# Kernel tuning notes

Measured on AMD Instinct MI355X. Metric: run time of the kernel, lower is better.

## Reference

```python
import jax, jax.numpy as jnp
import numpy as np

N, E = 10000, 160000
MUL0, MUL1, MUL2 = 64, 32, 16
DIM = MUL0 + MUL1 * 3 + MUL2 * 5          # 240
LAT, CPL, NTYPE = 128, 128, 95
NGATE = MUL1 + MUL2                        # 48 gate scalars
NCH = MUL0 + MUL1 + MUL2                   # 112 irrep channels
AVG_NEI = 16.0

# scaling_indices: per-channel index repeated over each irrep's dim
SCALE_IDX = np.concatenate([
    np.arange(MUL0),
    np.repeat(np.arange(MUL0, MUL0 + MUL1), 3),
    np.repeat(np.arange(MUL0 + MUL1, NCH), 5),
])


def _split(x, n):
    s = x[:, :MUL0]
    v1 = x[:, MUL0:MUL0 + MUL1 * 3].reshape(n, MUL1, 3)
    v2 = x[:, MUL0 + MUL1 * 3:].reshape(n, MUL2, 5)
    return s, v1, v2


def setup_inputs() -> dict:
    key = jax.random.key(0)
    ks = iter(jax.random.split(key, 48))
    rn = lambda *s: jax.random.normal(next(ks), s, dtype=jnp.float32)
    return dict(
        node_features=rn(N, DIM), edge_features=rn(E, DIM),
        latents=rn(E, LAT), msg_cpl=rn(N, CPL),
        node_onehot=jax.random.uniform(next(ks), (N, NTYPE), dtype=jnp.float32),
        wigner_D1=rn(E, 3, 3), wigner_D2=rn(E, 5, 5),
        so2_W0=rn(2 * MUL0, MUL0 + NGATE) * 0.08, so2_W1=rn(2 * MUL1, MUL1) * 0.12,
        so2_W2=rn(2 * MUL2, MUL2) * 0.17, so2_Ws=rn(LAT, NCH + NGATE) * 0.08,
        env_W=rn(LAT, NCH) * 0.08,
        post_W0=rn(MUL0, MUL0) * 0.12, post_b0=rn(MUL0) * 0.01,
        post_W1=rn(MUL1, MUL1) * 0.17, post_W2=rn(MUL2, MUL2) * 0.25,
        res_W0=rn(MUL0, MUL0) * 0.12, res_b0=rn(MUL0) * 0.01,
        res_W1=rn(MUL1, MUL1) * 0.17, res_W2=rn(MUL2, MUL2) * 0.25,
        cpl_W1=rn(CPL, CPL) * 0.08, cpl_b1=rn(CPL) * 0.01,
        cpl_W2=rn(CPL, NCH) * 0.08, cpl_b2=rn(NCH) * 0.01,
        gs_W=rn(MUL0, CPL) * 0.12, gs_b=rn(CPL) * 0.01,
        msg_W1=rn(2 * CPL, CPL) * 0.06, msg_b1=rn(CPL) * 0.01,
        msg_W2=rn(CPL, CPL) * 0.08, msg_b2=rn(CPL) * 0.01,
        ln_g=jnp.ones(CPL, jnp.float32), ln_b=jnp.zeros(CPL, jnp.float32),
        oh_w0=rn(MUL0, NTYPE) * 0.1, oh_w1=rn(MUL1, NTYPE) * 0.1, oh_w2=rn(MUL2, NTYPE) * 0.1,
        edge_index=jax.random.randint(next(ks), (2, E), 0, N),
    )


def _forward(node_features, edge_features, latents, msg_cpl, node_onehot,
             wigner_D1, wigner_D2, so2_W0, so2_W1, so2_W2, so2_Ws, env_W,
             post_W0, post_b0, post_W1, post_W2, res_W0, res_b0, res_W1, res_W2,
             cpl_W1, cpl_b1, cpl_W2, cpl_b2, gs_W, gs_b,
             msg_W1, msg_b1, msg_W2, msg_b2, ln_g, ln_b,
             oh_w0, oh_w1, oh_w2, edge_index):
    src = edge_index[0]
    ns, nv1, nv2 = _split(node_features, N)
    es, ev1, ev2 = _split(edge_features, E)
    # gather node feats to edges, concat with edge feats (per-l blocks)
    s_in = jnp.concatenate([ns[src], es], axis=1)                 # [E,128]
    v1_in = jnp.concatenate([nv1[src], ev1], axis=1)              # [E,64,3]
    v2_in = jnp.concatenate([nv2[src], ev2], axis=1)              # [E,32,5]
    # rotate into per-edge frame (Wigner D)
    v1_r = jnp.einsum('eij,ecj->eci', wigner_D1, v1_in)
    v2_r = jnp.einsum('eij,ecj->eci', wigner_D2, v2_in)
    # SO2 linear: shared channel mixing + latent-conditioned per-channel scales
    sc = latents @ so2_Ws                                         # [E,160]
    s_m = (s_in @ so2_W0) * sc[:, :MUL0 + NGATE]
    v1_m = jnp.einsum('eci,co->eoi', v1_r, so2_W1) * sc[:, MUL0 + NGATE:MUL0 + NGATE + MUL1, None]
    v2_m = jnp.einsum('eci,co->eoi', v2_r, so2_W2) * sc[:, MUL0 + NGATE + MUL1:, None]
    # rotate back
    v1_m = jnp.einsum('eji,eci->ecj', wigner_D1, v1_m)
    v2_m = jnp.einsum('eji,eci->ecj', wigner_D2, v2_m)
    # Gate activation
    s_act = jax.nn.silu(s_m[:, :MUL0])
    gates = jax.nn.sigmoid(s_m[:, MUL0:])
    v1_g = v1_m * gates[:, :MUL1, None]
    v2_g = v2_m * gates[:, MUL1:, None]
    # lin_post (per-l linear, bias on scalars)
    s_p = s_act @ post_W0 + post_b0
    v1_p = jnp.einsum('eci,co->eoi', v1_g, post_W1)
    v2_p = jnp.einsum('eci,co->eoi', v2_g, post_W2)
    # env element-wise weighting from latents
    w = latents @ env_W                                           # [E,112]
    s_p = s_p * w[:, :MUL0]
    v1_p = v1_p * w[:, MUL0:MUL0 + MUL1, None]
    v2_p = v2_p * w[:, MUL0 + MUL1:, None]
    msg = jnp.concatenate([s_p, v1_p.reshape(E, -1), v2_p.reshape(E, -1)], axis=1)
    # scatter-reduce to nodes + neighbor normalization
    agg = jax.ops.segment_sum(msg, src, num_segments=N) * (AVG_NEI ** -0.5)
    # coupling coefficients (per-channel, expanded by scaling_indices)
    coeffs = jax.nn.silu(msg_cpl @ cpl_W1 + cpl_b1) @ cpl_W2 + cpl_b2
    new_nf = agg * coeffs[:, SCALE_IDX]
    # coupling-channel update
    scal = new_nf[:, :MUL0] @ gs_W + gs_b
    h = jnp.concatenate([scal, msg_cpl], axis=1)
    upd = jax.nn.silu(h @ msg_W1 + msg_b1) @ msg_W2 + msg_b2
    mc = msg_cpl + upd
    mu = mc.mean(-1, keepdims=True)
    var = mc.var(-1, keepdims=True)
    msg_cpl_out = (mc - mu) * jax.lax.rsqrt(var + 1e-5) * ln_g + ln_b
    # residual mix with fixed logit-0 coefficients
    c = jax.nn.sigmoid(jnp.float32(0.0))
    c_old = jax.lax.rsqrt(c * c + 1.0)
    c_new = c * c_old
    rs = ns @ res_W0 + res_b0
    rv1 = jnp.einsum('eci,co->eoi', nv1, res_W1)
    rv2 = jnp.einsum('eci,co->eoi', nv2, res_W2)
    res = jnp.concatenate([rs, rv1.reshape(N, -1), rv2.reshape(N, -1)], axis=1)
    nf = c_new * new_nf + c_old * res
    # layer one-hot tensor product ('uvu' with 95x0e)
    inv = 1.0 / np.sqrt(NTYPE).astype(np.float32)
    g0 = (node_onehot @ oh_w0.T) * inv
    g1 = (node_onehot @ oh_w1.T) * inv
    g2 = (node_onehot @ oh_w2.T) * inv
    os_, ov1, ov2 = _split(nf, N)
    oh = jnp.concatenate([os_ * g0, (ov1 * g1[:, :, None]).reshape(N, -1),
                          (ov2 * g2[:, :, None]).reshape(N, -1)], axis=1)
    return nf + oh, msg_cpl_out


def reference(node_features, edge_features, latents, msg_cpl, node_onehot,
              wigner_D1, wigner_D2, so2_W0, so2_W1, so2_W2, so2_Ws, env_W,
              post_W0, post_b0, post_W1, post_W2, res_W0, res_b0, res_W1, res_W2,
              cpl_W1, cpl_b1, cpl_W2, cpl_b2, gs_W, gs_b,
              msg_W1, msg_b1, msg_W2, msg_b2, ln_g, ln_b,
              oh_w0, oh_w1, oh_w2, edge_index):
    return _forward(node_features, edge_features, latents, msg_cpl, node_onehot,
                    wigner_D1, wigner_D2, so2_W0, so2_W1, so2_W2, so2_Ws, env_W,
                    post_W0, post_b0, post_W1, post_W2, res_W0, res_b0, res_W1, res_W2,
                    cpl_W1, cpl_b1, cpl_W2, cpl_b2, gs_W, gs_b,
                    msg_W1, msg_b1, msg_W2, msg_b2, ln_g, ln_b,
                    oh_w0, oh_w1, oh_w2, edge_index)
```

## Files before the change

### kernel.cpp

```cpp
#include <hip/hip_runtime.h>

#define NN   10000
#define NE   160000
#define DIM  240
#define EB   16
#define NPB  16

typedef __bf16 bf16x8 __attribute__((ext_vector_type(8)));
typedef __bf16 bf16x4 __attribute__((ext_vector_type(4)));
typedef float  f32x4  __attribute__((ext_vector_type(4)));

__device__ __forceinline__ float sigf(float x) { return 1.0f / (1.0f + __expf(-x)); }

#define OFF_WB1 0
#define OFF_WB2 34816
#define OFF_W1  49152
#define OFF_W2  51200
#define OFF_PW0 51712
#define OFF_PW1 55808
#define OFF_PW2 56832
#define OHT_BYTE_OFF 131072
#define CNT_BYTE_OFF 196608
#define ROW_BYTE_OFF 237568
#define CUR_BYTE_OFF 282624
#define EID_BYTE_OFF 327680

__global__ __launch_bounds__(256) void prep_kernel(
    const float* __restrict__ Ws, const float* __restrict__ We, const float* __restrict__ W0,
    const float* __restrict__ W1, const float* __restrict__ W2,
    const float* __restrict__ pW0, const float* __restrict__ pW1, const float* __restrict__ pW2,
    const float* __restrict__ w0g, const float* __restrict__ w1g, const float* __restrict__ w2g,
    __bf16* __restrict__ wsb, float* __restrict__ ohT,
    const int* __restrict__ src, int* __restrict__ cnt)
{
    if (blockIdx.x >= 56) {
        if (cnt) {
            int e = (blockIdx.x - 56) * 256 + threadIdx.x;
            if (e < NE) atomicAdd(&cnt[src[e]], 1);
        }
        return;
    }
    int tid = blockIdx.x * 256 + threadIdx.x;
    const int stride = 56 * 256;
    for (int idx = tid; idx < 17*4*512; idx += stride) {
        int j = idx & 7, lane = (idx >> 3) & 63, ks = (idx >> 9) & 3, nt = idx >> 11;
        int k = ks*32 + (lane >> 4)*8 + j, n = nt*16 + (lane & 15);
        float v = (n < 160) ? Ws[k*160 + n] : We[k*112 + (n - 160)];
        wsb[OFF_WB1 + idx] = (__bf16)v;
    }
    for (int idx = tid; idx < 7*4*512; idx += stride) {
        int j = idx & 7, lane = (idx >> 3) & 63, ks = (idx >> 9) & 3, nt = idx >> 11;
        int k = ks*32 + (lane >> 4)*8 + j, n = nt*16 + (lane & 15);
        wsb[OFF_WB2 + idx] = (__bf16)W0[k*112 + n];
    }
    for (int idx = tid; idx < 2*2*512; idx += stride) {
        int j = idx & 7, lane = (idx >> 3) & 63, ks = (idx >> 9) & 1, nt = idx >> 10;
        int k = ks*32 + (lane >> 4)*8 + j, n = nt*16 + (lane & 15);
        wsb[OFF_W1 + idx] = (__bf16)W1[k*32 + n];
    }
    for (int idx = tid; idx < 512; idx += stride) {
        int j = idx & 7, lane = (idx >> 3) & 63;
        int k = (lane >> 4)*8 + j, n = lane & 15;
        wsb[OFF_W2 + idx] = (__bf16)W2[k*16 + n];
    }
    for (int idx = tid; idx < 4*2*512; idx += stride) {
        int j = idx & 7, lane = (idx >> 3) & 63, ks = (idx >> 9) & 1, nt = idx >> 10;
        int k = ks*32 + (lane >> 4)*8 + j, n = nt*16 + (lane & 15);
        wsb[OFF_PW0 + idx] = (__bf16)pW0[k*64 + n];
    }
    for (int idx = tid; idx < 2*512; idx += stride) {
        int j = idx & 7, lane = (idx >> 3) & 63, nt = idx >> 9;
        int k = (lane >> 4)*8 + j, n = nt*16 + (lane & 15);
        wsb[OFF_PW1 + idx] = (__bf16)pW1[k*32 + n];
    }
    for (int idx = tid; idx < 512; idx += stride) {
        int j = idx & 7, lane = (idx >> 3) & 63;
        int k = (lane >> 4)*8 + j, n = lane & 15;
        wsb[OFF_PW2 + idx] = (k < 16) ? (__bf16)pW2[k*16 + n] : (__bf16)0.0f;
    }
    for (int idx = tid; idx < 96*112; idx += stride) {
        int k = idx / 112, n2 = idx - k*112;
        float v = 0.f;
        if (k < 95) {
            if (n2 < 64)      v = w0g[n2*95 + k];
            else if (n2 < 96) v = w1g[(n2-64)*95 + k];
            else              v = w2g[(n2-96)*95 + k];
        }
        ohT[idx] = v * 0.10259783521f;
    }
}

__global__ __launch_bounds__(256) void scan_kernel(const int* __restrict__ cnt,
                                                   int* __restrict__ rowptr, int* __restrict__ cur) {
    __shared__ int part[256];
    int t = threadIdx.x;
    int base = t * 40;
    int local[40];
    int s = 0;
    #pragma unroll
    for (int i = 0; i < 40; i++) {
        int idx = base + i;
        int v = (idx < NN) ? cnt[idx] : 0;
        local[i] = s; s += v;
    }
    part[t] = s;
    __syncthreads();
    for (int off = 1; off < 256; off <<= 1) {
        int v = (t >= off) ? part[t - off] : 0;
        __syncthreads();
        part[t] += v;
        __syncthreads();
    }
    int pre = (t > 0) ? part[t - 1] : 0;
    #pragma unroll
    for (int i = 0; i < 40; i++) {
        int idx = base + i;
        if (idx < NN) { int r = pre + local[i]; rowptr[idx] = r; cur[idx] = r; }
    }
    if (t == 255) rowptr[NN] = part[255];
}

__global__ __launch_bounds__(256) void fill_kernel(const int* __restrict__ src,
                                                   int* __restrict__ cur, int* __restrict__ eidl) {
    int e = blockIdx.x * 256 + threadIdx.x;
    if (e < NE) {
        int slot = atomicAdd(&cur[src[e]], 1);
        eidl[slot] = e;
    }
}

__global__ __launch_bounds__(256, 4) void edge_mfma_kernel(
    const float* __restrict__ nf, const float* __restrict__ ef,
    const float* __restrict__ latg, const float* __restrict__ D1g, const float* __restrict__ D2g,
    const float* __restrict__ pb0, const int* __restrict__ srcg,
    const int* __restrict__ eidl, const __bf16* __restrict__ wsb, float* agg)
{
    __shared__ __align__(16) unsigned char pool[39936];
    __bf16* Cb   = (__bf16*)(pool + 0);
    __bf16* v1m  = (__bf16*)(pool + 12544);
    __bf16* v2m  = (__bf16*)(pool + 16384);
    __bf16* mtile= (__bf16*)(pool + 12544);
    __bf16* vt1  = (__bf16*)(pool + 20736);
    __bf16* vt2  = (__bf16*)(pool + 27136);
    __bf16* aV1g = (__bf16*)(pool + 20736);
    __bf16* aV2g = (__bf16*)(pool + 23808);
    float*  d1s  = (float*)(pool + 32512);
    float*  d2s  = (float*)(pool + 33088);
    __bf16* aSact= (__bf16*)(pool + 35648);
    float*  e1s  = (float*)(pool + 37696);
    float*  e2s  = (float*)(pool + 38272);
    int*    srcs = (int*)  (pool + 39872);

    const int t    = threadIdx.x;
    const int wid  = t >> 6, lane = t & 63;
    const int e0   = blockIdx.x * EB;

    #define EIDX(e) (eidl ? eidl[e0 + (e)] : (e0 + (e)))

    if (t < 16) srcs[t] = srcg[EIDX(t)];

    for (int idx = t; idx < 144; idx += 256) {
        int e = idx / 9; int ee = EIDX(e);
        d1s[idx] = D1g[(size_t)ee*9 + (idx - e*9)];
    }
    for (int idx = t; idx < 400; idx += 256) {
        int e = idx / 25; int ee = EIDX(e);
        d2s[idx] = D2g[(size_t)ee*25 + (idx - e*25)];
    }
    {
        int e = t >> 4, half = (t >> 3) & 1, cq = t & 7;
        int ee = EIDX(e);
        const float* base = half ? (ef + (size_t)ee*240 + 64 + cq*12)
                                 : (nf + (size_t)srcg[ee]*240 + 64 + cq*12);
        float4 f0 = *(const float4*)base;
        float4 f1 = *(const float4*)(base + 4);
        float4 f2 = *(const float4*)(base + 8);
        float f[12] = {f0.x,f0.y,f0.z,f0.w,f1.x,f1.y,f1.z,f1.w,f2.x,f2.y,f2.z,f2.w};
        int c = half*32 + cq*4;
        __bf16* dst = vt1 + e*200 + c;
        #pragma unroll
        for (int i = 0; i < 3; i++) {
            bf16x4 v = {(__bf16)f[i], (__bf16)f[3+i], (__bf16)f[6+i], (__bf16)f[9+i]};
            *(bf16x4*)(dst + i*64) = v;
        }
    }
    if (t < 128) {
        int e = t >> 3, half = (t >> 2) & 1, cq = t & 3;
        int ee = EIDX(e);
        const float* base = half ? (ef + (size_t)ee*240 + 160 + cq*20)
                                 : (nf + (size_t)srcg[ee]*240 + 160 + cq*20);
        float f[20];
        #pragma unroll
        for (int k = 0; k < 5; k++) {
            float4 q4 = *(const float4*)(base + k*4);
            f[4*k] = q4.x; f[4*k+1] = q4.y; f[4*k+2] = q4.z; f[4*k+3] = q4.w;
        }
        int c = half*16 + cq*4;
        __bf16* dst = vt2 + e*168 + c;
        #pragma unroll
        for (int z = 0; z < 5; z++) {
            bf16x4 v = {(__bf16)f[z], (__bf16)f[5+z], (__bf16)f[10+z], (__bf16)f[15+z]};
            *(bf16x4*)(dst + z*32) = v;
        }
    }

    {
        int col16 = lane & 15, ebase = (lane >> 4)*4;
        int e = lane & 15, q = lane >> 4;
        int ee = EIDX(e); int sn = srcg[ee];
        const float* latp = latg + (size_t)ee*128 + q*8;
        const float* nfp  = nf  + (size_t)sn*240 + q*8;
        const float* efp  = ef  + (size_t)ee*240 + q*8;
        bf16x8 aL[4], aS[4];
        #pragma unroll
        for (int ks = 0; ks < 4; ks++) {
            float4 f0 = *(const float4*)(latp + ks*32);
            float4 f1 = *(const float4*)(latp + ks*32 + 4);
            bf16x8 v;
            v[0]=(__bf16)f0.x; v[1]=(__bf16)f0.y; v[2]=(__bf16)f0.z; v[3]=(__bf16)f0.w;
            v[4]=(__bf16)f1.x; v[5]=(__bf16)f1.y; v[6]=(__bf16)f1.z; v[7]=(__bf16)f1.w;
            aL[ks] = v;
            const float* sp = (ks < 2) ? (nfp + ks*32) : (efp + (ks - 2)*32);
            float4 g0 = *(const float4*)sp;
            float4 g1 = *(const float4*)(sp + 4);
            bf16x8 w;
            w[0]=(__bf16)g0.x; w[1]=(__bf16)g0.y; w[2]=(__bf16)g0.z; w[3]=(__bf16)g0.w;
            w[4]=(__bf16)g1.x; w[5]=(__bf16)g1.y; w[6]=(__bf16)g1.z; w[7]=(__bf16)g1.w;
            aS[ks] = w;
        }
        #pragma unroll
        for (int it = 0; it < 6; it++) {
            int nt = wid + it*4;
            bool isLat = nt < 17;
            const __bf16* bB = isLat ? (wsb + OFF_WB1 + nt*2048)
                                     : (wsb + OFF_WB2 + (nt - 17)*2048);
            f32x4 acc = {0.f, 0.f, 0.f, 0.f};
            #pragma unroll
            for (int ks = 0; ks < 4; ks++) {
                bf16x8 b = *(const bf16x8*)(bB + (ks*64 + lane)*8);
                acc = __builtin_amdgcn_mfma_f32_16x16x32_bf16(isLat ? aL[ks] : aS[ks], b, acc, 0, 0, 0);
            }
            int col = (isLat ? nt*16 : 272 + (nt - 17)*16) + col16;
            #pragma unroll
            for (int r = 0; r < 4; r++) Cb[(ebase + r)*392 + col] = (__bf16)acc[r];
        }
    }
    __syncthreads();

    {
        int col16 = lane & 15, er = lane & 15, q8 = (lane >> 4)*8, ebase = (lane >> 4)*4;
        for (int p = wid; p < 11; p += 4) {
            f32x4 acc = {0.f, 0.f, 0.f, 0.f};
            if (p < 6) {
                int i = p >> 1, nt = p & 1;
                #pragma unroll
                for (int ks = 0; ks < 2; ks++) {
                    bf16x8 a = *(const bf16x8*)(vt1 + er*200 + i*64 + ks*32 + q8);
                    bf16x8 b = *(const bf16x8*)(wsb + OFF_W1 + ((nt*2 + ks)*64 + lane)*8);
                    acc = __builtin_amdgcn_mfma_f32_16x16x32_bf16(a, b, acc, 0, 0, 0);
                }
                int col = nt*16 + col16;
                #pragma unroll
                for (int r = 0; r < 4; r++) v1m[(i*16 + ebase + r)*40 + col] = (__bf16)acc[r];
            } else {
                int i = p - 6;
                bf16x8 a = *(const bf16x8*)(vt2 + er*168 + i*32 + q8);
                bf16x8 b = *(const bf16x8*)(wsb + OFF_W2 + lane*8);
                acc = __builtin_amdgcn_mfma_f32_16x16x32_bf16(a, b, acc, 0, 0, 0);
                #pragma unroll
                for (int r = 0; r < 4; r++) v2m[(i*16 + ebase + r)*24 + col16] = (__bf16)acc[r];
            }
        }
    }
    if (t < 128) {
        int ks = t >> 6, l2 = t & 63, e = l2 & 15, o0 = ks*32 + (l2 >> 4)*8;
        bf16x8 v;
        #pragma unroll
        for (int j = 0; j < 8; j++) {
            int o = o0 + j;
            float x = (float)Cb[e*392 + 272 + o] * (float)Cb[e*392 + o];
            v[j] = (__bf16)(x * sigf(x));
        }
        *(bf16x8*)(aSact + t*8) = v;
    }
    for (int idx = t; idx < 544; idx += 256) {
        if (idx < 144) {
            int e = idx / 9, r = idx - e*9, i = r / 3, k = r - i*3;
            const float* d = d1s + e*9;
            e1s[idx] = d[i*3+0]*d[0*3+k] + d[i*3+1]*d[1*3+k] + d[i*3+2]*d[2*3+k];
        } else {
            int j = idx - 144;
            int e = j / 25, r = j - e*25, i = r / 5, k = r - i*5;
            const float* d = d2s + e*25;
            float a = 0.f;
            #pragma unroll
            for (int tt = 0; tt < 5; tt++) a += d[i*5+tt] * d[tt*5+k];
            e2s[j] = a;
        }
    }
    __syncthreads();

    for (int idx = t; idx < 512; idx += 256) {
        if (idx < 192) {
            int i = idx >> 6, l2 = idx & 63, e = l2 & 15, c0 = (l2 >> 4)*8;
            float z0 = e1s[e*9 + i*3], z1 = e1s[e*9 + i*3 + 1], z2 = e1s[e*9 + i*3 + 2];
            bf16x8 m0 = *(const bf16x8*)(v1m + (0*16 + e)*40 + c0);
            bf16x8 m1 = *(const bf16x8*)(v1m + (1*16 + e)*40 + c0);
            bf16x8 m2 = *(const bf16x8*)(v1m + (2*16 + e)*40 + c0);
            bf16x8 s8 = *(const bf16x8*)(Cb + e*392 + 112 + c0);
            bf16x8 gA = *(const bf16x8*)(Cb + e*392 + 336 + c0);
            bf16x8 gB = *(const bf16x8*)(Cb + e*392 + 64 + c0);
            bf16x8 v;
            #pragma unroll
            for (int j = 0; j < 8; j++) {
                float g = sigf((float)gA[j] * (float)gB[j]);
                float a = z0*(float)m0[j] + z1*(float)m1[j] + z2*(float)m2[j];
                v[j] = (__bf16)(g * (float)s8[j] * a);
            }
            *(bf16x8*)(aV1g + idx*8) = v;
        } else {
            int idx2 = idx - 192;
            int i = idx2 >> 6, l2 = idx2 & 63, e = l2 & 15, c0 = (l2 >> 4)*8;
            bf16x8 v;
            if (c0 < 16) {
                const float* ee = e2s + e*25 + i*5;
                float z0 = ee[0], z1 = ee[1], z2 = ee[2], z3 = ee[3], z4 = ee[4];
                bf16x8 m0 = *(const bf16x8*)(v2m + (0*16 + e)*24 + c0);
                bf16x8 m1 = *(const bf16x8*)(v2m + (1*16 + e)*24 + c0);
                bf16x8 m2 = *(const bf16x8*)(v2m + (2*16 + e)*24 + c0);
                bf16x8 m3 = *(const bf16x8*)(v2m + (3*16 + e)*24 + c0);
                bf16x8 m4 = *(const bf16x8*)(v2m + (4*16 + e)*24 + c0);
                bf16x8 s8 = *(const bf16x8*)(Cb + e*392 + 144 + c0);
                bf16x8 gA = *(const bf16x8*)(Cb + e*392 + 368 + c0);
                bf16x8 gB = *(const bf16x8*)(Cb + e*392 + 96 + c0);
                #pragma unroll
                for (int j = 0; j < 8; j++) {
                    float g = sigf((float)gA[j] * (float)gB[j]);
                    float a = z0*(float)m0[j] + z1*(float)m1[j] + z2*(float)m2[j]
                            + z3*(float)m3[j] + z4*(float)m4[j];
                    v[j] = (__bf16)(g * (float)s8[j] * a);
                }
            } else {
                #pragma unroll
                for (int j = 0; j < 8; j++) v[j] = (__bf16)0.0f;
            }
            *(bf16x8*)(aV2g + idx2*8) = v;
        }
    }
    __syncthreads();

    {
        int col16 = lane & 15, ebase = (lane >> 4)*4;
        for (int p = wid; p < 15; p += 4) {
            f32x4 acc = {0.f, 0.f, 0.f, 0.f};
            if (p < 4) {
                int nt = p;
                #pragma unroll
                for (int ks = 0; ks < 2; ks++) {
                    bf16x8 a = *(const bf16x8*)(aSact + (ks*64 + lane)*8);
                    bf16x8 b = *(const bf16x8*)(wsb + OFF_PW0 + ((nt*2 + ks)*64 + lane)*8);
                    acc = __builtin_amdgcn_mfma_f32_16x16x32_bf16(a, b, acc, 0, 0, 0);
                }
                int o = nt*16 + col16;
                float bias = pb0[o];
                #pragma unroll
                for (int r = 0; r < 4; r++) {
                    int e = ebase + r;
                    float val = (acc[r] + bias) * (float)Cb[e*392 + 160 + o];
                    if (eidl) mtile[e*248 + o] = (__bf16)val;
                    else      atomicAdd(agg + (size_t)srcs[e]*240 + o, val);
                }
            } else if (p < 10) {
                int q = p - 4, i = q >> 1, nt = q & 1;
                bf16x8 a = *(const bf16x8*)(aV1g + (i*64 + lane)*8);
                bf16x8 b = *(const bf16x8*)(wsb + OFF_PW1 + (nt*64 + lane)*8);
                acc = __builtin_amdgcn_mfma_f32_16x16x32_bf16(a, b, acc, 0, 0, 0);
                int o = nt*16 + col16;
                #pragma unroll
                for (int r = 0; r < 4; r++) {
                    int e = ebase + r;
                    float val = acc[r] * (float)Cb[e*392 + 224 + o];
                    if (eidl) mtile[e*248 + 64 + o*3 + i] = (__bf16)val;
                    else      atomicAdd(agg + (size_t)srcs[e]*240 + 64 + o*3 + i, val);
                }
            } else {
                int i = p - 10;
                bf16x8 a = *(const bf16x8*)(aV2g + (i*64 + lane)*8);
                bf16x8 b = *(const bf16x8*)(wsb + OFF_PW2 + lane*8);
                acc = __builtin_amdgcn_mfma_f32_16x16x32_bf16(a, b, acc, 0, 0, 0);
                #pragma unroll
                for (int r = 0; r < 4; r++) {
                    int e = ebase + r;
                    float val = acc[r] * (float)Cb[e*392 + 256 + col16];
                    if (eidl) mtile[e*248 + 160 + col16*5 + i] = (__bf16)val;
                    else      atomicAdd(agg + (size_t)srcs[e]*240 + 160 + col16*5 + i, val);
                }
            }
        }
    }

    if (eidl) {
        __syncthreads();
        if (t < 240) {
            float s = 0.f;
            int prev = srcs[0];
            #pragma unroll
            for (int e = 0; e < EB; e++) {
                int sn = srcs[e];
                if (sn != prev) {
                    atomicAdd(agg + (size_t)prev*240 + t, s);
                    s = 0.f; prev = sn;
                }
                s += (float)mtile[e*248 + t];
            }
            atomicAdd(agg + (size_t)prev*240 + t, s);
        }
    }
    #undef EIDX
}

__global__ __launch_bounds__(256, 3) void node_kernel(
    const float* __restrict__ nf, const float* __restrict__ mcplg,
    const float* __restrict__ ohg,
    const float* __restrict__ cW1, const float* __restrict__ cb1,
    const float* __restrict__ cW2, const float* __restrict__ cb2,
    const float* __restrict__ gsW, const float* __restrict__ gsb,
    const float* __restrict__ mW1, const float* __restrict__ mb1,
    const float* __restrict__ mW2, const float* __restrict__ mb2,
    const float* __restrict__ lng, const float* __restrict__ lnb,
    const float* __restrict__ rW0, const float* __restrict__ rb0,
    const float* __restrict__ rW1, const float* __restrict__ rW2,
    const float* __restrict__ ohT, float* out0, float* out1)
{
    __shared__ __align__(16) unsigned char pool[53248];
    float* mcp  = (float*)(pool + 0);
    float* ohv  = (float*)(pool + 8192);
    float* anew = (float*)(pool + 14336);
    float* t12  = (float*)(pool + 29696);
    float* cfg  = (float*)(pool + 37888);
    float* scm  = (float*)(pool + 45056);

    const int t  = threadIdx.x;
    const int g  = t >> 7;
    const int o  = t & 127;
    const int nb = g * 8;
    const int n0 = blockIdx.x * NPB;

    for (int idx = t; idx < NPB * 128; idx += 256) {
        int n = idx >> 7, k = idx & 127;
        mcp[n*128 + k] = mcplg[(n0 + n) * 128 + k];
    }
    for (int idx = t; idx < NPB * 96; idx += 256) {
        int n = idx / 96, k = idx - n * 96;
        ohv[n*96 + k] = (k < 95) ? ohg[(n0 + n) * 95 + k] : 0.f;
    }
    for (int idx = t; idx < NPB * 240; idx += 256) {
        int n = idx / 240, k = idx - n * 240;
        anew[n*240 + k] = out0[(n0 + n) * DIM + k];
    }
    __syncthreads();

    {
        float a[8]; float b = cb1[o];
        #pragma unroll
        for (int i = 0; i < 8; i++) a[i] = b;
        #pragma unroll 2
        for (int k4 = 0; k4 < 32; k4++) {
            float w0 = cW1[(4*k4+0)*128 + o], w1 = cW1[(4*k4+1)*128 + o],
                  w2 = cW1[(4*k4+2)*128 + o], w3 = cW1[(4*k4+3)*128 + o];
            #pragma unroll
            for (int i = 0; i < 8; i++) {
                float4 m = *(const float4*)&mcp[(nb+i)*128 + 4*k4];
                a[i] += m.x*w0 + m.y*w1 + m.z*w2 + m.w*w3;
            }
        }
        #pragma unroll
        for (int i = 0; i < 8; i++) { float x = a[i]; t12[(nb+i)*128 + o] = x * sigf(x); }
    }
    __syncthreads();

    if (o < 112) {
        float a[8]; float b = cb2[o];
        #pragma unroll
        for (int i = 0; i < 8; i++) a[i] = b;
        #pragma unroll 2
        for (int k4 = 0; k4 < 32; k4++) {
            float w0 = cW2[(4*k4+0)*112 + o], w1 = cW2[(4*k4+1)*112 + o],
                  w2 = cW2[(4*k4+2)*112 + o], w3 = cW2[(4*k4+3)*112 + o];
            #pragma unroll
            for (int i = 0; i < 8; i++) {
                float4 m = *(const float4*)&t12[(nb+i)*128 + 4*k4];
                a[i] += m.x*w0 + m.y*w1 + m.z*w2 + m.w*w3;
            }
        }
        #pragma unroll
        for (int i = 0; i < 8; i++) cfg[(nb+i)*112 + o] = a[i];
    }
    __syncthreads();

    for (int idx = t; idx < NPB * 240; idx += 256) {
        int n = idx / 240, d = idx - n * 240;
        int ch = (d < 64) ? d : (d < 160 ? 64 + (d - 64) / 3 : 96 + (d - 160) / 5);
        anew[n*240 + d] *= 0.25f * cfg[n*112 + ch];
    }
    __syncthreads();

    {
        float a[8]; float b = gsb[o];
        #pragma unroll
        for (int i = 0; i < 8; i++) a[i] = b;
        #pragma unroll 2
        for (int k4 = 0; k4 < 16; k4++) {
            float w0 = gsW[(4*k4+0)*128 + o], w1 = gsW[(4*k4+1)*128 + o],
                  w2 = gsW[(4*k4+2)*128 + o], w3 = gsW[(4*k4+3)*128 + o];
            #pragma unroll
            for (int i = 0; i < 8; i++) {
                float4 m = *(const float4*)&anew[(nb+i)*240 + 4*k4];
                a[i] += m.x*w0 + m.y*w1 + m.z*w2 + m.w*w3;
            }
        }
        #pragma unroll
        for (int i = 0; i < 8; i++) scm[(nb+i)*128 + o] = a[i];
    }
    __syncthreads();

    {
        float a[8]; float b = mb1[o];
        #pragma unroll
        for (int i = 0; i < 8; i++) a[i] = b;
        #pragma unroll 2
        for (int k4 = 0; k4 < 32; k4++) {
            float w0 = mW1[(4*k4+0)*128 + o], w1 = mW1[(4*k4+1)*128 + o],
                  w2 = mW1[(4*k4+2)*128 + o], w3 = mW1[(4*k4+3)*128 + o];
            #pragma unroll
            for (int i = 0; i < 8; i++) {
                float4 m = *(const float4*)&scm[(nb+i)*128 + 4*k4];
                a[i] += m.x*w0 + m.y*w1 + m.z*w2 + m.w*w3;
            }
        }
        #pragma unroll 2
        for (int k4 = 0; k4 < 32; k4++) {
            float w0 = mW1[(128+4*k4+0)*128 + o], w1 = mW1[(128+4*k4+1)*128 + o],
                  w2 = mW1[(128+4*k4+2)*128 + o], w3 = mW1[(128+4*k4+3)*128 + o];
            #pragma unroll
            for (int i = 0; i < 8; i++) {
                float4 m = *(const float4*)&mcp[(nb+i)*128 + 4*k4];
                a[i] += m.x*w0 + m.y*w1 + m.z*w2 + m.w*w3;
            }
        }
        #pragma unroll
        for (int i = 0; i < 8; i++) { float x = a[i]; t12[(nb+i)*128 + o] = x * sigf(x); }
    }
    __syncthreads();

    {
        float a[8]; float b = mb2[o];
        #pragma unroll
        for (int i = 0; i < 8; i++) a[i] = b;
        #pragma unroll 2
        for (int k4 = 0; k4 < 32; k4++) {
            float w0 = mW2[(4*k4+0)*128 + o], w1 = mW2[(4*k4+1)*128 + o],
                  w2 = mW2[(4*k4+2)*128 + o], w3 = mW2[(4*k4+3)*128 + o];
            #pragma unroll
            for (int i = 0; i < 8; i++) {
                float4 m = *(const float4*)&t12[(nb+i)*128 + 4*k4];
                a[i] += m.x*w0 + m.y*w1 + m.z*w2 + m.w*w3;
            }
        }
        #pragma unroll
        for (int i = 0; i < 8; i++) scm[(nb+i)*128 + o] = mcp[(nb+i)*128 + o] + a[i];
    }
    __syncthreads();

    {
        int n = t >> 4, l = t & 15;
        float x[8]; float s = 0.f, ss = 0.f;
        #pragma unroll
        for (int i = 0; i < 8; i++) { x[i] = scm[n*128 + l + 16*i]; s += x[i]; ss += x[i]*x[i]; }
        #pragma unroll
        for (int off = 8; off > 0; off >>= 1) {
            s  += __shfl_down(s,  off, 16);
            ss += __shfl_down(ss, off, 16);
        }
        s  = __shfl(s, 0, 16);
        ss = __shfl(ss, 0, 16);
        float mu   = s * (1.f / 128.f);
        float var  = ss * (1.f / 128.f) - mu * mu;
        float rstd = rsqrtf(var + 1e-5f);
        float* op = out1 + (n0 + n) * 128;
        #pragma unroll
        for (int i = 0; i < 8; i++) {
            int c = l + 16*i;
            op[c] = (x[i] - mu) * rstd * lng[c] + lnb[c];
        }
    }

    if (o < 112) {
        float a[8] = {0.f,0.f,0.f,0.f,0.f,0.f,0.f,0.f};
        #pragma unroll 2
        for (int k4 = 0; k4 < 24; k4++) {
            float w0 = ohT[(4*k4+0)*112 + o], w1 = ohT[(4*k4+1)*112 + o],
                  w2 = ohT[(4*k4+2)*112 + o], w3 = ohT[(4*k4+3)*112 + o];
            #pragma unroll
            for (int i = 0; i < 8; i++) {
                float4 m = *(const float4*)&ohv[(nb+i)*96 + 4*k4];
                a[i] += m.x*w0 + m.y*w1 + m.z*w2 + m.w*w3;
            }
        }
        #pragma unroll
        for (int i = 0; i < 8; i++) cfg[(nb+i)*112 + o] = a[i];
    }
    __syncthreads();

    const float c_new = 0.4472135955f;
    const float c_old = 0.8944271910f;
    for (int idx = t; idx < NPB * 240; idx += 256) {
        int n = idx / 240, d = idx - n * 240;
        const float* nrow = nf + (size_t)(n0 + n) * DIM;
        float res, gg;
        if (d < 64) {
            float acc = rb0[d];
            #pragma unroll 4
            for (int c = 0; c < 64; c++) acc += nrow[c] * rW0[c * 64 + d];
            res = acc; gg = cfg[n*112 + d];
        } else if (d < 160) {
            int dd = d - 64, oo = dd / 3, j = dd - oo * 3;
            float acc = 0.f;
            #pragma unroll 4
            for (int c = 0; c < 32; c++) acc += nrow[64 + c*3 + j] * rW1[c * 32 + oo];
            res = acc; gg = cfg[n*112 + 64 + oo];
        } else {
            int dd = d - 160, oo = dd / 5, j = dd - oo * 5;
            float acc = 0.f;
            #pragma unroll 4
            for (int c = 0; c < 16; c++) acc += nrow[160 + c*5 + j] * rW2[c * 16 + oo];
            res = acc; gg = cfg[n*112 + 96 + oo];
        }
        float v = c_new * anew[n*240 + d] + c_old * res;
        out0[(n0 + n) * DIM + d] = v * (1.f + gg);
    }
}

extern "C" void kernel_launch(void* const* d_in, const int* in_sizes, int n_in,
                              void* d_out, int out_size, void* d_ws, size_t ws_size,
                              hipStream_t stream) {
    const float* nf      = (const float*)d_in[0];
    const float* ef      = (const float*)d_in[1];
    const float* lat     = (const float*)d_in[2];
    const float* mcpl    = (const float*)d_in[3];
    const float* ohot    = (const float*)d_in[4];
    const float* D1      = (const float*)d_in[5];
    const float* D2      = (const float*)d_in[6];
    const float* so2_W0  = (const float*)d_in[7];
    const float* so2_W1  = (const float*)d_in[8];
    const float* so2_W2  = (const float*)d_in[9];
    const float* so2_Ws  = (const float*)d_in[10];
    const float* env_W   = (const float*)d_in[11];
    const float* post_W0 = (const float*)d_in[12];
    const float* post_b0 = (const float*)d_in[13];
    const float* post_W1 = (const float*)d_in[14];
    const float* post_W2 = (const float*)d_in[15];
    const float* res_W0  = (const float*)d_in[16];
    const float* res_b0  = (const float*)d_in[17];
    const float* res_W1  = (const float*)d_in[18];
    const float* res_W2  = (const float*)d_in[19];
    const float* cpl_W1  = (const float*)d_in[20];
    const float* cpl_b1  = (const float*)d_in[21];
    const float* cpl_W2  = (const float*)d_in[22];
    const float* cpl_b2  = (const float*)d_in[23];
    const float* gs_W    = (const float*)d_in[24];
    const float* gs_b    = (const float*)d_in[25];
    const float* msg_W1  = (const float*)d_in[26];
    const float* msg_b1  = (const float*)d_in[27];
    const float* msg_W2  = (const float*)d_in[28];
    const float* msg_b2  = (const float*)d_in[29];
    const float* ln_g    = (const float*)d_in[30];
    const float* ln_b    = (const float*)d_in[31];
    const float* oh_w0   = (const float*)d_in[32];
    const float* oh_w1   = (const float*)d_in[33];
    const float* oh_w2   = (const float*)d_in[34];
    const int*   eidx    = (const int*)d_in[35];

    float* out0 = (float*)d_out;
    float* out1 = (float*)d_out + (size_t)NN * DIM;
    char*   wsB = (char*)d_ws;
    __bf16* wsb = (__bf16*)d_ws;
    float*  ohT = (float*)(wsB + OHT_BYTE_OFF);

    const size_t needA = (size_t)EID_BYTE_OFF + (size_t)NE * sizeof(int);
    const bool planA = ws_size >= needA;

    (void)hipMemsetAsync(out0, 0, (size_t)NN * DIM * sizeof(float), stream);

    if (planA) {
        int* cnt  = (int*)(wsB + CNT_BYTE_OFF);
        int* row  = (int*)(wsB + ROW_BYTE_OFF);
        int* cur  = (int*)(wsB + CUR_BYTE_OFF);
        int* eidl = (int*)(wsB + EID_BYTE_OFF);

        (void)hipMemsetAsync(cnt, 0, 10240 * sizeof(int), stream);
        prep_kernel<<<56 + (NE + 255) / 256, 256, 0, stream>>>(
            so2_Ws, env_W, so2_W0, so2_W1, so2_W2, post_W0, post_W1, post_W2,
            oh_w0, oh_w1, oh_w2, wsb, ohT, eidx, cnt);
        scan_kernel<<<1, 256, 0, stream>>>(cnt, row, cur);
        fill_kernel<<<(NE + 255) / 256, 256, 0, stream>>>(eidx, cur, eidl);

        edge_mfma_kernel<<<NE / EB, 256, 0, stream>>>(
            nf, ef, lat, D1, D2, post_b0, eidx, eidl, wsb, out0);
    } else {
        prep_kernel<<<56, 256, 0, stream>>>(
            so2_Ws, env_W, so2_W0, so2_W1, so2_W2, post_W0, post_W1, post_W2,
            oh_w0, oh_w1, oh_w2, wsb, ohT, eidx, nullptr);
        edge_mfma_kernel<<<NE / EB, 256, 0, stream>>>(
            nf, ef, lat, D1, D2, post_b0, eidx, nullptr, wsb, out0);
    }

    node_kernel<<<NN / NPB, 256, 0, stream>>>(
        nf, mcpl, ohot, cpl_W1, cpl_b1, cpl_W2, cpl_b2, gs_W, gs_b,
        msg_W1, msg_b1, msg_W2, msg_b2, ln_g, ln_b,
        res_W0, res_b0, res_W1, res_W2, ohT, out0, out1);
}
```

Before: 689.2 us.

## Halve edge tile to 8 edges per block with 128-thread blocks

```diff
diff --git a/kernel.cpp b/kernel.cpp
--- a/kernel.cpp
+++ b/kernel.cpp
@@ -3,7 +3,7 @@
 #define NN   10000
 #define NE   160000
 #define DIM  240
-#define EB   16
+#define EB   8
 #define NPB  16
 
 typedef __bf16 bf16x8 __attribute__((ext_vector_type(8)));
@@ -129,27 +129,27 @@
     }
 }
 
-__global__ __launch_bounds__(256, 4) void edge_mfma_kernel(
+__global__ __launch_bounds__(128, 4) void edge_mfma_kernel(
     const float* __restrict__ nf, const float* __restrict__ ef,
     const float* __restrict__ latg, const float* __restrict__ D1g, const float* __restrict__ D2g,
     const float* __restrict__ pb0, const int* __restrict__ srcg,
     const int* __restrict__ eidl, const __bf16* __restrict__ wsb, float* agg)
 {
-    __shared__ __align__(16) unsigned char pool[39936];
+    __shared__ __align__(16) unsigned char pool[20384];
     __bf16* Cb   = (__bf16*)(pool + 0);
-    __bf16* v1m  = (__bf16*)(pool + 12544);
-    __bf16* v2m  = (__bf16*)(pool + 16384);
-    __bf16* mtile= (__bf16*)(pool + 12544);
-    __bf16* vt1  = (__bf16*)(pool + 20736);
-    __bf16* vt2  = (__bf16*)(pool + 27136);
-    __bf16* aV1g = (__bf16*)(pool + 20736);
-    __bf16* aV2g = (__bf16*)(pool + 23808);
-    float*  d1s  = (float*)(pool + 32512);
-    float*  d2s  = (float*)(pool + 33088);
-    __bf16* aSact= (__bf16*)(pool + 35648);
-    float*  e1s  = (float*)(pool + 37696);
-    float*  e2s  = (float*)(pool + 38272);
-    int*    srcs = (int*)  (pool + 39872);
+    __bf16* v1m  = (__bf16*)(pool + 6272);
+    __bf16* v2m  = (__bf16*)(pool + 8192);
+    __bf16* mtile= (__bf16*)(pool + 6272);
+    __bf16* vt1  = (__bf16*)(pool + 10240);
+    __bf16* vt2  = (__bf16*)(pool + 13440);
+    __bf16* aV1g = (__bf16*)(pool + 10240);
+    __bf16* aV2g = (__bf16*)(pool + 13312);
+    float*  d1s  = (float*)(pool + 16128);
+    float*  d2s  = (float*)(pool + 16416);
+    float*  e1s  = (float*)(pool + 17216);
+    float*  e2s  = (float*)(pool + 17504);
+    __bf16* aSact= (__bf16*)(pool + 18304);
+    int*    srcs = (int*)  (pool + 20352);
 
     const int t    = threadIdx.x;
     const int wid  = t >> 6, lane = t & 63;
@@ -157,15 +157,15 @@
 
     #define EIDX(e) (eidl ? eidl[e0 + (e)] : (e0 + (e)))
 
-    if (t < 16) srcs[t] = srcg[EIDX(t)];
-
-    for (int idx = t; idx < 144; idx += 256) {
-        int e = idx / 9; int ee = EIDX(e);
-        d1s[idx] = D1g[(size_t)ee*9 + (idx - e*9)];
-    }
-    for (int idx = t; idx < 400; idx += 256) {
-        int e = idx / 25; int ee = EIDX(e);
-        d2s[idx] = D2g[(size_t)ee*25 + (idx - e*25)];
+    if (t < 8) srcs[t] = srcg[EIDX(t)];
+
+    for (int idx = t; idx < 72; idx += 128) {
+        int e = idx / 9;
+        d1s[idx] = D1g[(size_t)EIDX(e)*9 + (idx - e*9)];
+    }
+    for (int idx = t; idx < 200; idx += 128) {
+        int e = idx / 25;
+        d2s[idx] = D2g[(size_t)EIDX(e)*25 + (idx - e*25)];
     }
     {
         int e = t >> 4, half = (t >> 3) & 1, cq = t & 7;
@@ -184,7 +184,7 @@
             *(bf16x4*)(dst + i*64) = v;
         }
     }
-    if (t < 128) {
+    if (t < 64) {
         int e = t >> 3, half = (t >> 2) & 1, cq = t & 3;
         int ee = EIDX(e);
         const float* base = half ? (ef + (size_t)ee*240 + 160 + cq*20)
@@ -206,8 +206,8 @@
 
     {
         int col16 = lane & 15, ebase = (lane >> 4)*4;
-        int e = lane & 15, q = lane >> 4;
-        int ee = EIDX(e); int sn = srcg[ee];
+        int er = lane & 7, q = lane >> 4;
+        int ee = EIDX(er); int sn = srcg[ee];
         const float* latp = latg + (size_t)ee*128 + q*8;
         const float* nfp  = nf  + (size_t)sn*240 + q*8;
         const float* efp  = ef  + (size_t)ee*240 + q*8;
@@ -228,9 +228,9 @@
             w[4]=(__bf16)g1.x; w[5]=(__bf16)g1.y; w[6]=(__bf16)g1.z; w[7]=(__bf16)g1.w;
             aS[ks] = w;
         }
-        #pragma unroll
-        for (int it = 0; it < 6; it++) {
-            int nt = wid + it*4;
+        #pragma unroll 4
+        for (int it = 0; it < 12; it++) {
+            int nt = wid + it*2;
             bool isLat = nt < 17;
             const __bf16* bB = isLat ? (wsb + OFF_WB1 + nt*2048)
                                      : (wsb + OFF_WB2 + (nt - 17)*2048);
@@ -240,16 +240,18 @@
                 bf16x8 b = *(const bf16x8*)(bB + (ks*64 + lane)*8);
                 acc = __builtin_amdgcn_mfma_f32_16x16x32_bf16(isLat ? aL[ks] : aS[ks], b, acc, 0, 0, 0);
             }
-            int col = (isLat ? nt*16 : 272 + (nt - 17)*16) + col16;
-            #pragma unroll
-            for (int r = 0; r < 4; r++) Cb[(ebase + r)*392 + col] = (__bf16)acc[r];
-        }
-    }
-    __syncthreads();
-
-    {
-        int col16 = lane & 15, er = lane & 15, q8 = (lane >> 4)*8, ebase = (lane >> 4)*4;
-        for (int p = wid; p < 11; p += 4) {
+            if (ebase < 8) {
+                int col = (isLat ? nt*16 : 272 + (nt - 17)*16) + col16;
+                #pragma unroll
+                for (int r = 0; r < 4; r++) Cb[(ebase + r)*392 + col] = (__bf16)acc[r];
+            }
+        }
+    }
+    __syncthreads();
+
+    {
+        int col16 = lane & 15, er = lane & 7, q8 = (lane >> 4)*8, ebase = (lane >> 4)*4;
+        for (int p = wid; p < 11; p += 2) {
             f32x4 acc = {0.f, 0.f, 0.f, 0.f};
             if (p < 6) {
                 int i = p >> 1, nt = p & 1;
@@ -259,21 +261,25 @@
                     bf16x8 b = *(const bf16x8*)(wsb + OFF_W1 + ((nt*2 + ks)*64 + lane)*8);
                     acc = __builtin_amdgcn_mfma_f32_16x16x32_bf16(a, b, acc, 0, 0, 0);
                 }
-                int col = nt*16 + col16;
-                #pragma unroll
-                for (int r = 0; r < 4; r++) v1m[(i*16 + ebase + r)*40 + col] = (__bf16)acc[r];
+                if (ebase < 8) {
+                    int col = nt*16 + col16;
+                    #pragma unroll
+                    for (int r = 0; r < 4; r++) v1m[(i*8 + ebase + r)*40 + col] = (__bf16)acc[r];
+                }
             } else {
                 int i = p - 6;
                 bf16x8 a = *(const bf16x8*)(vt2 + er*168 + i*32 + q8);
                 bf16x8 b = *(const bf16x8*)(wsb + OFF_W2 + lane*8);
                 acc = __builtin_amdgcn_mfma_f32_16x16x32_bf16(a, b, acc, 0, 0, 0);
-                #pragma unroll
-                for (int r = 0; r < 4; r++) v2m[(i*16 + ebase + r)*24 + col16] = (__bf16)acc[r];
-            }
-        }
-    }
-    if (t < 128) {
-        int ks = t >> 6, l2 = t & 63, e = l2 & 15, o0 = ks*32 + (l2 >> 4)*8;
+                if (ebase < 8) {
+                    #pragma unroll
+                    for (int r = 0; r < 4; r++) v2m[(i*8 + ebase + r)*24 + col16] = (__bf16)acc[r];
+                }
+            }
+        }
+    }
+    {
+        int ks = t >> 6, l2 = t & 63, e = l2 & 7, o0 = ks*32 + (l2 >> 4)*8;
         bf16x8 v;
         #pragma unroll
         for (int j = 0; j < 8; j++) {
@@ -283,13 +289,13 @@
         }
         *(bf16x8*)(aSact + t*8) = v;
     }
-    for (int idx = t; idx < 544; idx += 256) {
-        if (idx < 144) {
+    for (int idx = t; idx < 272; idx += 128) {
+        if (idx < 72) {
             int e = idx / 9, r = idx - e*9, i = r / 3, k = r - i*3;
             const float* d = d1s + e*9;
             e1s[idx] = d[i*3+0]*d[0*3+k] + d[i*3+1]*d[1*3+k] + d[i*3+2]*d[2*3+k];
         } else {
-            int j = idx - 144;
+            int j = idx - 72;
             int e = j / 25, r = j - e*25, i = r / 5, k = r - i*5;
             const float* d = d2s + e*25;
             float a = 0.f;
@@ -300,13 +306,13 @@
     }
     __syncthreads();
 
-    for (int idx = t; idx < 512; idx += 256) {
+    for (int idx = t; idx < 512; idx += 128) {
         if (idx < 192) {
-            int i = idx >> 6, l2 = idx & 63, e = l2 & 15, c0 = (l2 >> 4)*8;
+            int i = idx >> 6, l2 = idx & 63, e = l2 & 7, c0 = (l2 >> 4)*8;
             float z0 = e1s[e*9 + i*3], z1 = e1s[e*9 + i*3 + 1], z2 = e1s[e*9 + i*3 + 2];
-            bf16x8 m0 = *(const bf16x8*)(v1m + (0*16 + e)*40 + c0);
-            bf16x8 m1 = *(const bf16x8*)(v1m + (1*16 + e)*40 + c0);
-            bf16x8 m2 = *(const bf16x8*)(v1m + (2*16 + e)*40 + c0);
+            bf16x8 m0 = *(const bf16x8*)(v1m + (0*8 + e)*40 + c0);
+            bf16x8 m1 = *(const bf16x8*)(v1m + (1*8 + e)*40 + c0);
+            bf16x8 m2 = *(const bf16x8*)(v1m + (2*8 + e)*40 + c0);
             bf16x8 s8 = *(const bf16x8*)(Cb + e*392 + 112 + c0);
             bf16x8 gA = *(const bf16x8*)(Cb + e*392 + 336 + c0);
             bf16x8 gB = *(const bf16x8*)(Cb + e*392 + 64 + c0);
@@ -320,19 +326,19 @@
             *(bf16x8*)(aV1g + idx*8) = v;
         } else {
             int idx2 = idx - 192;
-            int i = idx2 >> 6, l2 = idx2 & 63, e = l2 & 15, c0 = (l2 >> 4)*8;
-            bf16x8 v;
-            if (c0 < 16) {
+            int i = idx2 >> 6, l2 = idx2 & 63, e = l2 & 7, q = l2 >> 4, c0 = q*8;
+            if (q < 2) {
                 const float* ee = e2s + e*25 + i*5;
                 float z0 = ee[0], z1 = ee[1], z2 = ee[2], z3 = ee[3], z4 = ee[4];
-                bf16x8 m0 = *(const bf16x8*)(v2m + (0*16 + e)*24 + c0);
-                bf16x8 m1 = *(const bf16x8*)(v2m + (1*16 + e)*24 + c0);
-                bf16x8 m2 = *(const bf16x8*)(v2m + (2*16 + e)*24 + c0);
-                bf16x8 m3 = *(const bf16x8*)(v2m + (3*16 + e)*24 + c0);
-                bf16x8 m4 = *(const bf16x8*)(v2m + (4*16 + e)*24 + c0);
+                bf16x8 m0 = *(const bf16x8*)(v2m + (0*8 + e)*24 + c0);
+                bf16x8 m1 = *(const bf16x8*)(v2m + (1*8 + e)*24 + c0);
+                bf16x8 m2 = *(const bf16x8*)(v2m + (2*8 + e)*24 + c0);
+                bf16x8 m3 = *(const bf16x8*)(v2m + (3*8 + e)*24 + c0);
+                bf16x8 m4 = *(const bf16x8*)(v2m + (4*8 + e)*24 + c0);
                 bf16x8 s8 = *(const bf16x8*)(Cb + e*392 + 144 + c0);
                 bf16x8 gA = *(const bf16x8*)(Cb + e*392 + 368 + c0);
                 bf16x8 gB = *(const bf16x8*)(Cb + e*392 + 96 + c0);
+                bf16x8 v;
                 #pragma unroll
                 for (int j = 0; j < 8; j++) {
                     float g = sigf((float)gA[j] * (float)gB[j]);
@@ -340,18 +346,15 @@
                             + z3*(float)m3[j] + z4*(float)m4[j];
                     v[j] = (__bf16)(g * (float)s8[j] * a);
                 }
-            } else {
-                #pragma unroll
-                for (int j = 0; j < 8; j++) v[j] = (__bf16)0.0f;
-            }
-            *(bf16x8*)(aV2g + idx2*8) = v;
-        }
-    }
-    __syncthreads();
-
-    {
-        int col16 = lane & 15, ebase = (lane >> 4)*4;
-        for (int p = wid; p < 15; p += 4) {
+                *(bf16x8*)(aV2g + (i*32 + q*16 + (l2 & 15))*8) = v;
+            }
+        }
+    }
+    __syncthreads();
+
+    {
+        int col16 = lane & 15, ebase = (lane >> 4)*4, q4 = lane >> 4;
+        for (int p = wid; p < 15; p += 2) {
             f32x4 acc = {0.f, 0.f, 0.f, 0.f};
             if (p < 4) {
                 int nt = p;
@@ -361,39 +364,48 @@
                     bf16x8 b = *(const bf16x8*)(wsb + OFF_PW0 + ((nt*2 + ks)*64 + lane)*8);
                     acc = __builtin_amdgcn_mfma_f32_16x16x32_bf16(a, b, acc, 0, 0, 0);
                 }
-                int o = nt*16 + col16;
-                float bias = pb0[o];
-                #pragma unroll
-                for (int r = 0; r < 4; r++) {
-                    int e = ebase + r;
-                    float val = (acc[r] + bias) * (float)Cb[e*392 + 160 + o];
-                    if (eidl) mtile[e*248 + o] = (__bf16)val;
-                    else      atomicAdd(agg + (size_t)srcs[e]*240 + o, val);
+                if (ebase < 8) {
+                    int o = nt*16 + col16;
+                    float bias = pb0[o];
+                    #pragma unroll
+                    for (int r = 0; r < 4; r++) {
+                        int e = ebase + r;
+                        float val = (acc[r] + bias) * (float)Cb[e*392 + 160 + o];
+                        if (eidl) mtile[e*248 + o] = (__bf16)val;
+                        else      atomicAdd(agg + (size_t)srcs[e]*240 + o, val);
+                    }
                 }
             } else if (p < 10) {
                 int q = p - 4, i = q >> 1, nt = q & 1;
                 bf16x8 a = *(const bf16x8*)(aV1g + (i*64 + lane)*8);
                 bf16x8 b = *(const bf16x8*)(wsb + OFF_PW1 + (nt*64 + lane)*8);
                 acc = __builtin_amdgcn_mfma_f32_16x16x32_bf16(a, b, acc, 0, 0, 0);
-                int o = nt*16 + col16;
-                #pragma unroll
-                for (int r = 0; r < 4; r++) {
-                    int e = ebase + r;
-                    float val = acc[r] * (float)Cb[e*392 + 224 + o];
-                    if (eidl) mtile[e*248 + 64 + o*3 + i] = (__bf16)val;
-                    else      atomicAdd(agg + (size_t)srcs[e]*240 + 64 + o*3 + i, val);
+                if (ebase < 8) {
+                    int o = nt*16 + col16;
+                    #pragma unroll
+                    for (int r = 0; r < 4; r++) {
+                        int e = ebase + r;
+                        float val = acc[r] * (float)Cb[e*392 + 224 + o];
+                        if (eidl) mtile[e*248 + 64 + o*3 + i] = (__bf16)val;
+                        else      atomicAdd(agg + (size_t)srcs[e]*240 + 64 + o*3 + i, val);
+                    }
                 }
             } else {
                 int i = p - 10;
-                bf16x8 a = *(const bf16x8*)(aV2g + (i*64 + lane)*8);
+                bf16x8 a;
+                #pragma unroll
+                for (int j = 0; j < 8; j++) a[j] = (__bf16)0.0f;
+                if (q4 < 2) a = *(const bf16x8*)(aV2g + (i*32 + q4*16 + col16)*8);
                 bf16x8 b = *(const bf16x8*)(wsb + OFF_PW2 + lane*8);
                 acc = __builtin_amdgcn_mfma_f32_16x16x32_bf16(a, b, acc, 0, 0, 0);
-                #pragma unroll
-                for (int r = 0; r < 4; r++) {
-                    int e = ebase + r;
-                    float val = acc[r] * (float)Cb[e*392 + 256 + col16];
-                    if (eidl) mtile[e*248 + 160 + col16*5 + i] = (__bf16)val;
-                    else      atomicAdd(agg + (size_t)srcs[e]*240 + 160 + col16*5 + i, val);
+                if (ebase < 8) {
+                    #pragma unroll
+                    for (int r = 0; r < 4; r++) {
+                        int e = ebase + r;
+                        float val = acc[r] * (float)Cb[e*392 + 256 + col16];
+                        if (eidl) mtile[e*248 + 160 + col16*5 + i] = (__bf16)val;
+                        else      atomicAdd(agg + (size_t)srcs[e]*240 + 160 + col16*5 + i, val);
+                    }
                 }
             }
         }
@@ -401,19 +413,19 @@
 
     if (eidl) {
         __syncthreads();
-        if (t < 240) {
+        for (int d = t; d < 240; d += 128) {
             float s = 0.f;
             int prev = srcs[0];
             #pragma unroll
             for (int e = 0; e < EB; e++) {
                 int sn = srcs[e];
                 if (sn != prev) {
-                    atomicAdd(agg + (size_t)prev*240 + t, s);
+                    atomicAdd(agg + (size_t)prev*240 + d, s);
                     s = 0.f; prev = sn;
                 }
-                s += (float)mtile[e*248 + t];
-            }
-            atomicAdd(agg + (size_t)prev*240 + t, s);
+                s += (float)mtile[e*248 + d];
+            }
+            atomicAdd(agg + (size_t)prev*240 + d, s);
         }
     }
     #undef EIDX
@@ -705,13 +717,13 @@
         scan_kernel<<<1, 256, 0, stream>>>(cnt, row, cur);
         fill_kernel<<<(NE + 255) / 256, 256, 0, stream>>>(eidx, cur, eidl);
 
-        edge_mfma_kernel<<<NE / EB, 256, 0, stream>>>(
+        edge_mfma_kernel<<<NE / EB, 128, 0, stream>>>(
             nf, ef, lat, D1, D2, post_b0, eidx, eidl, wsb, out0);
     } else {
         prep_kernel<<<56, 256, 0, stream>>>(
             so2_Ws, env_W, so2_W0, so2_W1, so2_W2, post_W0, post_W1, post_W2,
             oh_w0, oh_w1, oh_w2, wsb, ohT, eidx, nullptr);
-        edge_mfma_kernel<<<NE / EB, 256, 0, stream>>>(
+        edge_mfma_kernel<<<NE / EB, 128, 0, stream>>>(
             nf, ef, lat, D1, D2, post_b0, eidx, nullptr, wsb, out0);
     }
 
```

Result: slower. 801.0 us (+16.2%).
